# Optimization experiments

Measured on AMD Instinct MI355X. Metric: run time of the kernel, lower is better.

The kernel has to match this reference:

```python
import jax, jax.numpy as jnp
import numpy as np
from jax import lax

B, DIM, L = 8, 512, 4096
GROUPS, NQ, CSIZE = 2, 8, 1024
DG = DIM // GROUPS


def setup_inputs() -> dict:
    key = jax.random.key(0)
    ks = jax.random.split(key, 10)
    s = 0.02
    return {
        "x": jax.random.normal(ks[0], (B, DIM, L), dtype=jnp.float32),
        "conv_enc_w": jax.random.normal(ks[1], (DIM, DIM, 3), dtype=jnp.float32) * s,
        "conv_enc_b": jnp.zeros((DIM,), jnp.float32),
        "pre_w": jax.random.normal(ks[2], (DIM, DIM), dtype=jnp.float32) * s,
        "pre_b": jnp.zeros((DIM,), jnp.float32),
        "codebooks": jax.random.normal(ks[3], (NQ, GROUPS, CSIZE, DG), dtype=jnp.float32) * s,
        "post_w": jax.random.normal(ks[4], (DIM, DIM), dtype=jnp.float32) * s,
        "post_b": jnp.zeros((DIM,), jnp.float32),
        "conv_dec_w": jax.random.normal(ks[5], (DIM, DIM, 3), dtype=jnp.float32) * s,
        "conv_dec_b": jnp.zeros((DIM,), jnp.float32),
    }


def _conv1d(x, w, b):
    # x: [b, d, l], w: [out, in, k], 'same' padding for k=3
    y = lax.conv_general_dilated(x, w, window_strides=(1,), padding=((1, 1),),
                                 dimension_numbers=("NCH", "OIH", "NCH"))
    return y + b[None, :, None]


def _grouped_residual_vq(h, codebooks):
    # h: [b, l, G, dg], codebooks: [Q, G, C, dg]
    b, l, g, dg = h.shape
    gidx = jnp.arange(g)[None, None, :]

    def step(carry, cb):
        residual, qout = carry
        # squared-euclidean argmin (||r||^2 term dropped: constant over codes)
        dots = jnp.einsum("blgd,gcd->blgc", residual, cb)
        c2 = jnp.sum(cb * cb, axis=-1)  # [g, c]
        idx = jnp.argmin(c2[None, None] - 2.0 * dots, axis=-1)  # [b, l, g]
        quant = cb[gidx, idx]  # gather -> [b, l, g, dg]
        commit = jnp.mean((residual - lax.stop_gradient(quant)) ** 2, axis=(0, 1, 3))  # [g]
        quant_st = residual + lax.stop_gradient(quant - residual)  # straight-through
        return (residual - lax.stop_gradient(quant), qout + quant_st), (idx, commit)

    (_, qout), (all_idx, all_loss) = lax.scan(step, (h, jnp.zeros_like(h)), codebooks)
    # all_idx: [Q, b, l, G] -> [G, b, l, Q]; all_loss: [Q, G] -> [G, Q]
    return qout, all_idx.transpose(3, 1, 2, 0), all_loss.T


def reference(x, conv_enc_w, conv_enc_b, pre_w, pre_b, codebooks,
              post_w, post_b, conv_dec_w, conv_dec_b):
    b, d, l = x.shape
    g = codebooks.shape[1]
    h = _conv1d(x, conv_enc_w, conv_enc_b)            # [b, d, l]
    h = h.transpose(0, 2, 1)                          # [b, l, d]
    h = h @ pre_w.T + pre_b                           # pre linear
    hg = h.reshape(b, l, g, d // g)                   # chunk dim into groups
    qout, indices, losses = _grouped_residual_vq(hg, codebooks)
    q = qout.reshape(b, l, d) @ post_w.T + post_b     # post linear
    q = q.transpose(0, 2, 1)                          # [b, d, l]
    _ = _conv1d(q, conv_dec_w, conv_dec_b)            # computed then discarded, as in original
    return (q, indices, losses)
```

## Files before the change

kernel.cpp:

```cpp
#include <hip/hip_runtime.h>
#include <cstdint>
#include <cstddef>

#define BB     8
#define DIMC   512
#define LL     4096
#define POSN   (BB*LL)
#define NG     2
#define NQ     8
#define CS     1024
#define DG     256

#define Q_OFF    0
#define IDX_OFF  16777216
#define LOSS_OFF 17301504

#define OFF_WFT   0
#define OFF_BF    786432
#define OFF_C2    786944
#define OFF_QOUT  803328
#define OFF_CANDD 17580544
#define OFF_CANDI 17842688
#define OFF_LOSSP 18104832

__global__ __launch_bounds__(256) void k_fuse_w(const float* __restrict__ cw,
                                               const float* __restrict__ prew,
                                               float* __restrict__ wft) {
    __shared__ __align__(16) float As[16][68];
    __shared__ __align__(16) float Bs[16][68];
    int bid = blockIdx.x;
    int mt = bid >> 3, nt = bid & 7;
    int m0 = mt * 64, n0 = nt * 64;
    int t = threadIdx.x, tx = t & 15, ty = t >> 4;
    float acc[4][4] = {};
    for (int k0 = 0; k0 < 512; k0 += 16) {
        for (int u = t; u < 16 * 64; u += 256) {
            int kk = u >> 6, mm = u & 63;
            As[kk][mm] = cw[(size_t)(k0 + kk) * 1536 + m0 + mm];
        }
        {
            int r = t >> 2, c4 = t & 3;
            float4 v = *(const float4*)&prew[(size_t)(n0 + r) * 512 + k0 + c4 * 4];
            Bs[c4 * 4 + 0][r] = v.x; Bs[c4 * 4 + 1][r] = v.y;
            Bs[c4 * 4 + 2][r] = v.z; Bs[c4 * 4 + 3][r] = v.w;
        }
        __syncthreads();
#pragma unroll
        for (int k = 0; k < 16; ++k) {
            float4 a = *(const float4*)&As[k][ty * 4];
            float4 b = *(const float4*)&Bs[k][tx * 4];
            float av[4] = {a.x, a.y, a.z, a.w}, bv[4] = {b.x, b.y, b.z, b.w};
#pragma unroll
            for (int i = 0; i < 4; ++i)
#pragma unroll
                for (int j = 0; j < 4; ++j) acc[i][j] += av[i] * bv[j];
        }
        __syncthreads();
    }
#pragma unroll
    for (int i = 0; i < 4; ++i) {
        float4 v = {acc[i][0], acc[i][1], acc[i][2], acc[i][3]};
        *(float4*)&wft[(size_t)(m0 + ty * 4 + i) * 512 + n0 + tx * 4] = v;
    }
}

__global__ void k_bias(const float* __restrict__ prew, const float* __restrict__ preb,
                       const float* __restrict__ ceb, float* __restrict__ bf) {
    int dd = blockIdx.x * 256 + threadIdx.x;
    if (dd < 512) {
        float s = preb[dd];
        for (int j = 0; j < 512; ++j) s += prew[(size_t)dd * 512 + j] * ceb[j];
        bf[dd] = s;
    }
}

__global__ void k_c2(const float* __restrict__ cb, float* __restrict__ c2) {
    int wave = threadIdx.x >> 6, lane = threadIdx.x & 63;
    int row = blockIdx.x * 4 + wave;
    const float* r = cb + (size_t)row * 256;
    float4 v = *(const float4*)&r[lane * 4];
    float s = v.x * v.x + v.y * v.y + v.z * v.z + v.w * v.w;
#pragma unroll
    for (int m = 1; m < 64; m <<= 1) s += __shfl_xor(s, m);
    if (lane == 0) c2[row] = s;
}

__global__ __launch_bounds__(256) void k_conv(const float* __restrict__ x,
                                              const float* __restrict__ wft,
                                              const float* __restrict__ bf,
                                              float* __restrict__ h) {
    int bid = blockIdx.x;
    int dt = bid >> 9;
    int rem = bid & 511;
    int bb = rem >> 6, lt = rem & 63;
    int l0 = lt * 64, d0 = dt * 64;
    int t = threadIdx.x, tx = t & 15, ty = t >> 4;
    __shared__ float Xs[8][68];
    __shared__ __align__(16) float Ws[24][64];
    float acc[4][4] = {};
    const float* xb = x + (size_t)bb * 512 * 4096;
    for (int i0 = 0; i0 < 512; i0 += 8) {
        for (int u = t; u < 8 * 66; u += 256) {
            int ii = u / 66, c = u % 66;
            int gl = l0 + c - 1;
            Xs[ii][c] = (gl >= 0 && gl < 4096) ? xb[(size_t)(i0 + ii) * 4096 + gl] : 0.f;
        }
        for (int u = t; u < 24 * 64; u += 256) {
            int r = u >> 6, c = u & 63;
            Ws[r][c] = wft[(size_t)(i0 * 3 + r) * 512 + d0 + c];
        }
        __syncthreads();
#pragma unroll
        for (int ii = 0; ii < 8; ++ii) {
            float a[6];
#pragma unroll
            for (int j = 0; j < 6; ++j) a[j] = Xs[ii][ty * 4 + j];
#pragma unroll
            for (int k = 0; k < 3; ++k) {
                float4 b = *(const float4*)&Ws[ii * 3 + k][tx * 4];
                float bv[4] = {b.x, b.y, b.z, b.w};
#pragma unroll
                for (int jl = 0; jl < 4; ++jl)
#pragma unroll
                    for (int jd = 0; jd < 4; ++jd) acc[jl][jd] += a[jl + k] * bv[jd];
            }
        }
        __syncthreads();
    }
    int posb = bb * 4096 + l0 + ty * 4;
    const float4 bias = *(const float4*)&bf[d0 + tx * 4];
#pragma unroll
    for (int jl = 0; jl < 4; ++jl) {
        float4 v = {acc[jl][0] + bias.x, acc[jl][1] + bias.y,
                    acc[jl][2] + bias.z, acc[jl][3] + bias.w};
        *(float4*)&h[(size_t)(posb + jl) * 512 + d0 + tx * 4] = v;
    }
}

__global__ __launch_bounds__(256) void k_dots(const float* __restrict__ hres,
                                              const float* __restrict__ cb,
                                              const float* __restrict__ c2,
                                              float* __restrict__ candd,
                                              int* __restrict__ candi,
                                              int q, int g) {
    __shared__ __align__(16) float As[16][132];
    __shared__ __align__(16) float Bs[16][132];
    __shared__ float Dd[16][128];
    __shared__ int   Di[16][128];
    int bid = blockIdx.x;
    int mt = bid >> 3, nt = bid & 7;
    int p0 = mt * 128, n0 = nt * 128;
    int t = threadIdx.x, pt = t & 15, ct = t >> 4;
    const float* cbq = cb + (size_t)(q * 2 + g) * 1024 * 256;
    const float* c2q = c2 + (q * 2 + g) * 1024;
    float acc[8][8] = {};
    for (int k0 = 0; k0 < 256; k0 += 16) {
        for (int u = t; u < 128 * 4; u += 256) {
            int r = u >> 2, c4 = u & 3;
            float4 v = *(const float4*)&hres[(size_t)(p0 + r) * 512 + g * 256 + k0 + c4 * 4];
            As[c4 * 4 + 0][r] = v.x; As[c4 * 4 + 1][r] = v.y;
            As[c4 * 4 + 2][r] = v.z; As[c4 * 4 + 3][r] = v.w;
        }
        for (int u = t; u < 128 * 4; u += 256) {
            int r = u >> 2, c4 = u & 3;
            float4 v = *(const float4*)&cbq[(size_t)(n0 + r) * 256 + k0 + c4 * 4];
            Bs[c4 * 4 + 0][r] = v.x; Bs[c4 * 4 + 1][r] = v.y;
            Bs[c4 * 4 + 2][r] = v.z; Bs[c4 * 4 + 3][r] = v.w;
        }
        __syncthreads();
#pragma unroll
        for (int k = 0; k < 16; ++k) {
            float4 a0 = *(const float4*)&As[k][pt * 8];
            float4 a1 = *(const float4*)&As[k][pt * 8 + 4];
            float4 b0 = *(const float4*)&Bs[k][ct * 8];
            float4 b1 = *(const float4*)&Bs[k][ct * 8 + 4];
            float av[8] = {a0.x, a0.y, a0.z, a0.w, a1.x, a1.y, a1.z, a1.w};
            float bv[8] = {b0.x, b0.y, b0.z, b0.w, b1.x, b1.y, b1.z, b1.w};
#pragma unroll
            for (int i = 0; i < 8; ++i)
#pragma unroll
                for (int j = 0; j < 8; ++j) acc[i][j] += av[i] * bv[j];
        }
        __syncthreads();
    }
#pragma unroll
    for (int i = 0; i < 8; ++i) {
        float bd = 1e30f; int bi = 0x7fffffff;
#pragma unroll
        for (int j = 0; j < 8; ++j) {
            int c = n0 + ct * 8 + j;
            float d = c2q[c] - 2.f * acc[i][j];
            if (d < bd) { bd = d; bi = c; }
        }
        Dd[ct][pt * 8 + i] = bd;
        Di[ct][pt * 8 + i] = bi;
    }
    __syncthreads();
    if (t < 128) {
        float bd = Dd[0][t]; int bi = Di[0][t];
#pragma unroll
        for (int j = 1; j < 16; ++j) {
            float d = Dd[j][t]; int i2 = Di[j][t];
            if (d < bd || (d == bd && i2 < bi)) { bd = d; bi = i2; }
        }
        candd[(size_t)(p0 + t) * 8 + nt] = bd;
        candi[(size_t)(p0 + t) * 8 + nt] = bi;
    }
}

__global__ __launch_bounds__(256) void k_fin(float* __restrict__ hres,
                                             const float* __restrict__ cb,
                                             const float* __restrict__ candd,
                                             const int* __restrict__ candi,
                                             float* __restrict__ qout,
                                             float* __restrict__ lossp,
                                             float* __restrict__ idx_out,
                                             int q, int g) {
    int t = threadIdx.x, wave = t >> 6, lane = t & 63;
    const float* cbq = cb + (size_t)(q * 2 + g) * 1024 * 256;
    float lsum = 0.f;
    int pbase = blockIdx.x * 32 + wave * 8;
    for (int i = 0; i < 8; ++i) {
        int pos = pbase + i;
        float bd; int bi;
        if (lane < 8) { bd = candd[(size_t)pos * 8 + lane]; bi = candi[(size_t)pos * 8 + lane]; }
        else          { bd = 1e30f; bi = 0x7fffffff; }
#pragma unroll
        for (int m = 1; m < 8; m <<= 1) {
            float d2 = __shfl_xor(bd, m);
            int   i2 = __shfl_xor(bi, m);
            if (d2 < bd || (d2 == bd && i2 < bi)) { bd = d2; bi = i2; }
        }
        int idx = __shfl(bi, 0);
        float4 cv = *(const float4*)&cbq[(size_t)idx * 256 + lane * 4];
        size_t ro = (size_t)pos * 512 + g * 256 + lane * 4;
        float4 rv = *(const float4*)&hres[ro];
        float4 rn = {rv.x - cv.x, rv.y - cv.y, rv.z - cv.z, rv.w - cv.w};
        *(float4*)&hres[ro] = rn;
        if (q == 0) {
            *(float4*)&qout[ro] = cv;
        } else {
            float4 qv = *(const float4*)&qout[ro];
            qv.x += cv.x; qv.y += cv.y; qv.z += cv.z; qv.w += cv.w;
            *(float4*)&qout[ro] = qv;
        }
        lsum += rn.x * rn.x + rn.y * rn.y + rn.z * rn.z + rn.w * rn.w;
        if (lane == 0)
            idx_out[(size_t)(g * 32768 + pos) * 8 + q] = (float)idx;
    }
#pragma unroll
    for (int m = 1; m < 64; m <<= 1) lsum += __shfl_xor(lsum, m);
    __shared__ float ls[4];
    if (lane == 0) ls[wave] = lsum;
    __syncthreads();
    if (t == 0) lossp[(size_t)(g * 8 + q) * 1024 + blockIdx.x] = ls[0] + ls[1] + ls[2] + ls[3];
}

__global__ __launch_bounds__(256) void k_post(const float* __restrict__ qout,
                                              const float* __restrict__ pw,
                                              const float* __restrict__ pb,
                                              float* __restrict__ out) {
    __shared__ __align__(16) float As[16][68];
    __shared__ __align__(16) float Bs[16][68];
    int bid = blockIdx.x;
    int mt = bid >> 3, nt = bid & 7;
    int p0 = mt * 64, d0 = nt * 64;
    int t = threadIdx.x, tx = t & 15, ty = t >> 4;
    float acc[4][4] = {};
    for (int k0 = 0; k0 < 512; k0 += 16) {
        int r = t >> 2, c4 = t & 3;
        {
            float4 v = *(const float4*)&qout[(size_t)(p0 + r) * 512 + k0 + c4 * 4];
            As[c4 * 4 + 0][r] = v.x; As[c4 * 4 + 1][r] = v.y;
            As[c4 * 4 + 2][r] = v.z; As[c4 * 4 + 3][r] = v.w;
        }
        {
            float4 v = *(const float4*)&pw[(size_t)(d0 + r) * 512 + k0 + c4 * 4];
            Bs[c4 * 4 + 0][r] = v.x; Bs[c4 * 4 + 1][r] = v.y;
            Bs[c4 * 4 + 2][r] = v.z; Bs[c4 * 4 + 3][r] = v.w;
        }
        __syncthreads();
#pragma unroll
        for (int k = 0; k < 16; ++k) {
            float4 a = *(const float4*)&As[k][tx * 4];
            float4 b = *(const float4*)&Bs[k][ty * 4];
            float av[4] = {a.x, a.y, a.z, a.w}, bv[4] = {b.x, b.y, b.z, b.w};
#pragma unroll
            for (int i = 0; i < 4; ++i)
#pragma unroll
                for (int j = 0; j < 4; ++j) acc[i][j] += av[i] * bv[j];
        }
        __syncthreads();
    }
    int bb = p0 >> 12, l0 = p0 & 4095;
#pragma unroll
    for (int jd = 0; jd < 4; ++jd) {
        int dd = d0 + ty * 4 + jd;
        float bias = pb[dd];
        float4 v = {acc[0][jd] + bias, acc[1][jd] + bias,
                    acc[2][jd] + bias, acc[3][jd] + bias};
        *(float4*)&out[((size_t)bb * 512 + dd) * 4096 + l0 + tx * 4] = v;
    }
}

__global__ void k_lossfin(const float* __restrict__ lossp, float* __restrict__ out) {
    int gq = blockIdx.x;
    float s = 0.f;
    for (int u = threadIdx.x; u < 1024; u += 256) s += lossp[(size_t)gq * 1024 + u];
    int wave = threadIdx.x >> 6, lane = threadIdx.x & 63;
#pragma unroll
    for (int m = 1; m < 64; m <<= 1) s += __shfl_xor(s, m);
    __shared__ float sh[4];
    if (lane == 0) sh[wave] = s;
    __syncthreads();
    if (threadIdx.x == 0)
        out[gq] = (sh[0] + sh[1] + sh[2] + sh[3]) * (1.f / (8.f * 4096.f * 256.f));
}

extern "C" void kernel_launch(void* const* d_in, const int* in_sizes, int n_in,
                              void* d_out, int out_size, void* d_ws, size_t ws_size,
                              hipStream_t stream) {
    (void)in_sizes; (void)n_in; (void)out_size; (void)ws_size;
    const float* x     = (const float*)d_in[0];
    const float* cew   = (const float*)d_in[1];
    const float* ceb   = (const float*)d_in[2];
    const float* prew  = (const float*)d_in[3];
    const float* preb  = (const float*)d_in[4];
    const float* cb    = (const float*)d_in[5];
    const float* postw = (const float*)d_in[6];
    const float* postb = (const float*)d_in[7];

    float* out = (float*)d_out;
    float* ws  = (float*)d_ws;
    float* wft   = ws + OFF_WFT;
    float* bf    = ws + OFF_BF;
    float* c2    = ws + OFF_C2;
    float* qout  = ws + OFF_QOUT;
    float* candd = ws + OFF_CANDD;
    int*   candi = (int*)(ws + OFF_CANDI);
    float* lossp = ws + OFF_LOSSP;
    float* h = out;

    k_fuse_w<<<192, 256, 0, stream>>>(cew, prew, wft);
    k_bias<<<2, 256, 0, stream>>>(prew, preb, ceb, bf);
    k_c2<<<4096, 256, 0, stream>>>(cb, c2);
    k_conv<<<4096, 256, 0, stream>>>(x, wft, bf, h);
    for (int q = 0; q < 8; ++q) {
        for (int g = 0; g < 2; ++g) {
            k_dots<<<2048, 256, 0, stream>>>(h, cb, c2, candd, candi, q, g);
            k_fin<<<1024, 256, 0, stream>>>(h, cb, candd, candi, qout, lossp,
                                            out + IDX_OFF, q, g);
        }
    }
    k_post<<<4096, 256, 0, stream>>>(qout, postw, postb, out);
    k_lossfin<<<16, 256, 0, stream>>>(lossp, out + LOSS_OFF);
}
```

Measured before the change: 4.924 ms.

## Use split-fp16 MFMA for post linear and rebuild qout from indices

```diff
diff --git a/kernel.cpp b/kernel.cpp
--- a/kernel.cpp
+++ b/kernel.cpp
@@ -18,10 +18,38 @@
 #define OFF_WFT   0
 #define OFF_BF    786432
 #define OFF_C2    786944
-#define OFF_QOUT  803328
+#define OFF_QH    803328
 #define OFF_CANDD 17580544
 #define OFF_CANDI 17842688
 #define OFF_LOSSP 18104832
+#define OFF_PWH   18121216
+
+typedef _Float16 f16;
+typedef _Float16 f16x8 __attribute__((ext_vector_type(8)));
+typedef _Float16 f16x4 __attribute__((ext_vector_type(4)));
+typedef float f32x4 __attribute__((ext_vector_type(4)));
+
+#define LO_SCALE      1024.f
+#define LO_INV        (1.f/1024.f)
+#define F16_MIN_NORM  6.103515625e-05f
+
+struct f16pair { f16 h, l; };
+
+__device__ __forceinline__ f16pair split1(float v) {
+    f16 hv = (f16)v;
+    float hf = (float)hv;
+    if (__builtin_fabsf(hf) < F16_MIN_NORM) { hv = (f16)0.f; hf = 0.f; }
+    f16pair p;
+    p.h = hv;
+    p.l = (f16)((v - hf) * LO_SCALE);
+    return p;
+}
+
+__device__ __forceinline__ void gload16(const void* g, void* l) {
+    __builtin_amdgcn_global_load_lds(
+        (const __attribute__((address_space(1))) void*)g,
+        (__attribute__((address_space(3))) void*)l, 16, 0, 0);
+}
 
 __global__ __launch_bounds__(256) void k_fuse_w(const float* __restrict__ cw,
                                                const float* __restrict__ prew,
@@ -83,6 +111,20 @@
 #pragma unroll
     for (int m = 1; m < 64; m <<= 1) s += __shfl_xor(s, m);
     if (lane == 0) c2[row] = s;
+}
+
+__global__ void k_split_pw(const float* __restrict__ pw, f16* __restrict__ ph,
+                           f16* __restrict__ pl) {
+    size_t i = ((size_t)blockIdx.x * 256 + threadIdx.x) * 4;
+    float4 v = *(const float4*)&pw[i];
+    f16x4 hv, lv;
+    f16pair p0 = split1(v.x), p1 = split1(v.y), p2 = split1(v.z), p3 = split1(v.w);
+    hv.x = p0.h; lv.x = p0.l;
+    hv.y = p1.h; lv.y = p1.l;
+    hv.z = p2.h; lv.z = p2.l;
+    hv.w = p3.h; lv.w = p3.l;
+    *(f16x4*)&ph[i] = hv;
+    *(f16x4*)&pl[i] = lv;
 }
 
 __global__ __launch_bounds__(256) void k_conv(const float* __restrict__ x,
@@ -212,7 +254,6 @@
                                              const float* __restrict__ cb,
                                              const float* __restrict__ candd,
                                              const int* __restrict__ candi,
-                                             float* __restrict__ qout,
                                              float* __restrict__ lossp,
                                              float* __restrict__ idx_out,
                                              int q, int g) {
@@ -237,13 +278,6 @@
         float4 rv = *(const float4*)&hres[ro];
         float4 rn = {rv.x - cv.x, rv.y - cv.y, rv.z - cv.z, rv.w - cv.w};
         *(float4*)&hres[ro] = rn;
-        if (q == 0) {
-            *(float4*)&qout[ro] = cv;
-        } else {
-            float4 qv = *(const float4*)&qout[ro];
-            qv.x += cv.x; qv.y += cv.y; qv.z += cv.z; qv.w += cv.w;
-            *(float4*)&qout[ro] = qv;
-        }
         lsum += rn.x * rn.x + rn.y * rn.y + rn.z * rn.z + rn.w * rn.w;
         if (lane == 0)
             idx_out[(size_t)(g * 32768 + pos) * 8 + q] = (float)idx;
@@ -256,50 +290,99 @@
     if (t == 0) lossp[(size_t)(g * 8 + q) * 1024 + blockIdx.x] = ls[0] + ls[1] + ls[2] + ls[3];
 }
 
-__global__ __launch_bounds__(256) void k_post(const float* __restrict__ qout,
-                                              const float* __restrict__ pw,
-                                              const float* __restrict__ pb,
-                                              float* __restrict__ out) {
-    __shared__ __align__(16) float As[16][68];
-    __shared__ __align__(16) float Bs[16][68];
+__global__ __launch_bounds__(256) void k_qsum2(const float* __restrict__ idxf,
+                                               const float* __restrict__ cb,
+                                               f16* __restrict__ qh,
+                                               f16* __restrict__ ql) {
+    int t = threadIdx.x, w = t >> 6, lane = t & 63;
+    int pair = blockIdx.x * 4 + w;
+    int g = pair & 1, pos = pair >> 1;
+    const float* ip = idxf + ((size_t)g * 32768 + pos) * 8;
+    float4 s = {0.f, 0.f, 0.f, 0.f};
+    for (int qq = 0; qq < 8; ++qq) {
+        int ii = (int)ip[qq];
+        const float* rowp = cb + ((size_t)(qq * 2 + g) * 1024 + ii) * 256;
+        float4 v = *(const float4*)&rowp[lane * 4];
+        s.x += v.x; s.y += v.y; s.z += v.z; s.w += v.w;
+    }
+    f16x4 hv, lv;
+    f16pair p0 = split1(s.x), p1 = split1(s.y), p2 = split1(s.z), p3 = split1(s.w);
+    hv.x = p0.h; lv.x = p0.l;
+    hv.y = p1.h; lv.y = p1.l;
+    hv.z = p2.h; lv.z = p2.l;
+    hv.w = p3.h; lv.w = p3.l;
+    size_t o = (size_t)pos * 512 + g * 256 + lane * 4;
+    *(f16x4*)&qh[o] = hv;
+    *(f16x4*)&ql[o] = lv;
+}
+
+__global__ __launch_bounds__(256) void k_post_mfma(const f16* __restrict__ qh,
+                                                   const f16* __restrict__ ql,
+                                                   const f16* __restrict__ pwh,
+                                                   const f16* __restrict__ pwl,
+                                                   const float* __restrict__ pb,
+                                                   float* __restrict__ out) {
+    __shared__ __align__(16) f16 Ah[4096], Al[4096], Bh[4096], Bl[4096];
     int bid = blockIdx.x;
-    int mt = bid >> 3, nt = bid & 7;
-    int p0 = mt * 64, d0 = nt * 64;
-    int t = threadIdx.x, tx = t & 15, ty = t >> 4;
-    float acc[4][4] = {};
-    for (int k0 = 0; k0 < 512; k0 += 16) {
-        int r = t >> 2, c4 = t & 3;
-        {
-            float4 v = *(const float4*)&qout[(size_t)(p0 + r) * 512 + k0 + c4 * 4];
-            As[c4 * 4 + 0][r] = v.x; As[c4 * 4 + 1][r] = v.y;
-            As[c4 * 4 + 2][r] = v.z; As[c4 * 4 + 3][r] = v.w;
-        }
-        {
-            float4 v = *(const float4*)&pw[(size_t)(d0 + r) * 512 + k0 + c4 * 4];
-            Bs[c4 * 4 + 0][r] = v.x; Bs[c4 * 4 + 1][r] = v.y;
-            Bs[c4 * 4 + 2][r] = v.z; Bs[c4 * 4 + 3][r] = v.w;
-        }
-        __syncthreads();
-#pragma unroll
-        for (int k = 0; k < 16; ++k) {
-            float4 a = *(const float4*)&As[k][tx * 4];
-            float4 b = *(const float4*)&Bs[k][ty * 4];
-            float av[4] = {a.x, a.y, a.z, a.w}, bv[4] = {b.x, b.y, b.z, b.w};
-#pragma unroll
-            for (int i = 0; i < 4; ++i)
-#pragma unroll
-                for (int j = 0; j < 4; ++j) acc[i][j] += av[i] * bv[j];
-        }
+    int mt = bid >> 2, nt = bid & 3;
+    int p0 = mt << 7, d0 = nt << 7;
+    int t = threadIdx.x, w = t >> 6, lane = t & 63;
+    int wm = (w >> 1) * 64, wn = (w & 1) * 64;
+    const f16* gA;
+    f16* lA;
+    {
+        const f16* a0 = qh + (size_t)p0 * 512;
+        const f16* a1 = ql + (size_t)p0 * 512;
+        const f16* b0 = pwh + (size_t)d0 * 512;
+        const f16* b1 = pwl + (size_t)d0 * 512;
+        gA = (w == 0) ? a0 : (w == 1) ? a1 : (w == 2) ? b0 : b1;
+        lA = (w == 0) ? Ah : (w == 1) ? Al : (w == 2) ? Bh : Bl;
+    }
+    f32x4 acc[4][4] = {};
+    f32x4 acc2[4][4] = {};
+    int lr = lane & 15, kq = lane >> 4;
+    for (int k0 = 0; k0 < 512; k0 += 32) {
+#pragma unroll
+        for (int u = 0; u < 8; ++u) {
+            int kb = u >> 1, hf = u & 1;
+            gload16(gA + (size_t)(hf * 64 + lane) * 512 + k0 + kb * 8,
+                    lA + kb * 1024 + hf * 512);
+        }
+        __syncthreads();
+        f16x8 a_h[4], a_l[4], b_h[4], b_l[4];
+#pragma unroll
+        for (int i = 0; i < 4; ++i) {
+            int ao = kq * 1024 + (wm + i * 16 + lr) * 8;
+            int bo = kq * 1024 + (wn + i * 16 + lr) * 8;
+            a_h[i] = *(const f16x8*)&Ah[ao];
+            a_l[i] = *(const f16x8*)&Al[ao];
+            b_h[i] = *(const f16x8*)&Bh[bo];
+            b_l[i] = *(const f16x8*)&Bl[bo];
+        }
+#pragma unroll
+        for (int i = 0; i < 4; ++i)
+#pragma unroll
+            for (int j = 0; j < 4; ++j) {
+                acc[i][j]  = __builtin_amdgcn_mfma_f32_16x16x32_f16(a_h[i], b_h[j], acc[i][j], 0, 0, 0);
+                acc2[i][j] = __builtin_amdgcn_mfma_f32_16x16x32_f16(a_h[i], b_l[j], acc2[i][j], 0, 0, 0);
+                acc2[i][j] = __builtin_amdgcn_mfma_f32_16x16x32_f16(a_l[i], b_h[j], acc2[i][j], 0, 0, 0);
+            }
         __syncthreads();
     }
     int bb = p0 >> 12, l0 = p0 & 4095;
 #pragma unroll
-    for (int jd = 0; jd < 4; ++jd) {
-        int dd = d0 + ty * 4 + jd;
+    for (int nj = 0; nj < 4; ++nj) {
+        int dd = d0 + wn + nj * 16 + lr;
         float bias = pb[dd];
-        float4 v = {acc[0][jd] + bias, acc[1][jd] + bias,
-                    acc[2][jd] + bias, acc[3][jd] + bias};
-        *(float4*)&out[((size_t)bb * 512 + dd) * 4096 + l0 + tx * 4] = v;
+        float* orow = out + ((size_t)bb * 512 + dd) * 4096 + l0 + wm + kq * 4;
+#pragma unroll
+        for (int mi = 0; mi < 4; ++mi) {
+            f32x4 v;
+#pragma unroll
+            for (int rg = 0; rg < 4; ++rg)
+                v[rg] = acc[mi][nj][rg] + acc2[mi][nj][rg] * LO_INV + bias;
+            *(f32x4*)&orow[mi * 16] = v;
+        }
     }
 }
 
@@ -335,23 +418,28 @@
     float* wft   = ws + OFF_WFT;
     float* bf    = ws + OFF_BF;
     float* c2    = ws + OFF_C2;
-    float* qout  = ws + OFF_QOUT;
+    f16*   qh    = (f16*)(ws + OFF_QH);
+    f16*   ql    = qh + 16777216;
     float* candd = ws + OFF_CANDD;
     int*   candi = (int*)(ws + OFF_CANDI);
     float* lossp = ws + OFF_LOSSP;
-    float* h = out;
+    f16*   pwh   = (f16*)(ws + OFF_PWH);
+    f16*   pwl   = pwh + 262144;
+    float* hres = out;
 
     k_fuse_w<<<192, 256, 0, stream>>>(cew, prew, wft);
     k_bias<<<2, 256, 0, stream>>>(prew, preb, ceb, bf);
     k_c2<<<4096, 256, 0, stream>>>(cb, c2);
-    k_conv<<<4096, 256, 0, stream>>>(x, wft, bf, h);
+    k_split_pw<<<256, 256, 0, stream>>>(postw, pwh, pwl);
+    k_conv<<<4096, 256, 0, stream>>>(x, wft, bf, hres);
     for (int q = 0; q < 8; ++q) {
         for (int g = 0; g < 2; ++g) {
-            k_dots<<<2048, 256, 0, stream>>>(h, cb, c2, candd, candi, q, g);
-            k_fin<<<1024, 256, 0, stream>>>(h, cb, candd, candi, qout, lossp,
+            k_dots<<<2048, 256, 0, stream>>>(hres, cb, c2, candd, candi, q, g);
+            k_fin<<<1024, 256, 0, stream>>>(hres, cb, candd, candi, lossp,
                                             out + IDX_OFF, q, g);
         }
     }
-    k_post<<<4096, 256, 0, stream>>>(qout, postw, postb, out);
+    k_qsum2<<<16384, 256, 0, stream>>>(out + IDX_OFF, cb, qh, ql);
+    k_post_mfma<<<1024, 256, 0, stream>>>(qh, ql, pwh, pwl, postb, out);
     k_lossfin<<<16, 256, 0, stream>>>(lossp, out + LOSS_OFF);
 }
```

Result: faster. 4.777 ms (-3.0%).
